# Kernel tuning notes

Hardware: AMD Instinct MI355X
Metric: run time of the kernel (lower is better)

## Reference

```python
import jax, jax.numpy as jnp
import numpy as np

B, S, D_MODEL, H = 2, 2048, 1024, 16
HD = D_MODEL // H  # 64
EPS = 1e-6


def setup_inputs() -> dict:
    key = jax.random.key(0)
    ks = jax.random.split(key, 8)
    x = jax.random.normal(ks[0], (B, S, D_MODEL), dtype=jnp.float32)
    # Proper RoPE rotation angles: theta_i = pos / 10000^(2i/head_dim)
    inv_freq = 1.0 / (10000.0 ** (np.arange(0, HD, 2, dtype=np.float32) / HD))  # (HD/2,)
    angles = np.arange(S, dtype=np.float32)[:, None] * inv_freq[None, :]        # (S, HD/2)
    rope_cos = jnp.asarray(np.cos(angles))
    rope_sin = jnp.asarray(np.sin(angles))
    w_std = 1.0 / np.sqrt(D_MODEL)
    wq = jax.random.normal(ks[1], (D_MODEL, D_MODEL), dtype=jnp.float32) * w_std
    wk = jax.random.normal(ks[2], (D_MODEL, D_MODEL), dtype=jnp.float32) * w_std
    wv = jax.random.normal(ks[3], (D_MODEL, D_MODEL), dtype=jnp.float32) * w_std
    wo = jax.random.normal(ks[4], (D_MODEL, D_MODEL), dtype=jnp.float32) * w_std
    q_scale = 1.0 + 0.02 * jax.random.normal(ks[5], (HD,), dtype=jnp.float32)
    k_scale = 1.0 + 0.02 * jax.random.normal(ks[6], (HD,), dtype=jnp.float32)
    return {"x": x, "wq": wq, "wk": wk, "wv": wv, "wo": wo,
            "q_scale": q_scale, "k_scale": k_scale,
            "rope_cos": rope_cos, "rope_sin": rope_sin}


def _rmsnorm(t, scale):
    # RMSNorm over head_dim
    var = jnp.mean(jnp.square(t), axis=-1, keepdims=True)
    return t * jax.lax.rsqrt(var + EPS) * scale


def _apply_rope(t, cos, sin):
    # t: (B,S,H,HD); interpret consecutive pairs as complex (real, imag)
    b, s, h, d = t.shape
    tp = t.reshape(b, s, h, d // 2, 2)
    tr, ti = tp[..., 0], tp[..., 1]
    c = cos[None, :, None, :]  # (1,S,1,HD/2)
    sn = sin[None, :, None, :]
    or_ = tr * c - ti * sn
    oi = tr * sn + ti * c
    return jnp.stack([or_, oi], axis=-1).reshape(b, s, h, d)


def reference(x, wq, wk, wv, wo, q_scale, k_scale, rope_cos, rope_sin):
    b, s, _ = x.shape
    # Torch-style linear: y = x @ W^T, W is (out, in)
    q = jnp.einsum('bsd,od->bso', x, wq).reshape(b, s, H, HD)
    k = jnp.einsum('bsd,od->bso', x, wk).reshape(b, s, H, HD)
    v = jnp.einsum('bsd,od->bso', x, wv).reshape(b, s, H, HD)
    q = _apply_rope(_rmsnorm(q, q_scale), rope_cos, rope_sin)
    k = _apply_rope(_rmsnorm(k, k_scale), rope_cos, rope_sin)
    # scaled dot-product attention (no mask), fp32 softmax
    scale = 1.0 / np.sqrt(HD)
    scores = jnp.einsum('bqhd,bkhd->bhqk', q, k) * scale
    probs = jax.nn.softmax(scores.astype(jnp.float32), axis=-1)
    attn = jnp.einsum('bhqk,bkhd->bqhd', probs, v).reshape(b, s, D_MODEL)
    return jnp.einsum('bso,do->bsd', attn, wo.T).astype(x.dtype) if False else jnp.einsum('bsd,od->bso', attn, wo)
```

## Files before the change

### kernel.cpp

```cpp
#include <hip/hip_runtime.h>
#include <hip/hip_bf16.h>


#define B_ 2
#define S_ 2048
#define D_ 1024
#define H_ 16
#define HD_ 64
#define M_ (B_*S_)
#define SPLIT_ 2
#define KSPAN_ (S_/SPLIT_)

typedef __attribute__((ext_vector_type(8))) short short8;
typedef __attribute__((ext_vector_type(4))) short short4v;
typedef __attribute__((ext_vector_type(4))) float f32x4;
typedef __attribute__((ext_vector_type(4))) _Float16 half4;
typedef __attribute__((ext_vector_type(8))) _Float16 half8;

static __device__ __forceinline__ short f2bf(float f) {
    __hip_bfloat16 h = __float2bfloat16(f);
    return *reinterpret_cast<short*>(&h);
}
static __device__ __forceinline__ short f2h(float f) {
    _Float16 h = (_Float16)f;
    return *reinterpret_cast<short*>(&h);
}

typedef __attribute__((address_space(1))) const unsigned int gu32_t;
typedef __attribute__((address_space(3))) unsigned int lu32_t;
static __device__ __forceinline__ void gld16(const short* g, short* l) {
    __builtin_amdgcn_global_load_lds((gu32_t*)g, (lu32_t*)l, 16, 0, 0);
}

__global__ __launch_bounds__(256)
void convert_bf16(const float* __restrict__ x,
                  const float* __restrict__ wq, const float* __restrict__ wk,
                  const float* __restrict__ wv, const float* __restrict__ wo,
                  short* __restrict__ xb, short* __restrict__ wqkvb, short* __restrict__ wob)
{
    const size_t t4 = ((size_t)blockIdx.x * 256 + threadIdx.x) * 4;
    const float* src; short* dst; size_t off, doff;
    if (t4 < 4194304)      { src = x;  dst = xb;    off = t4;           doff = t4; }
    else if (t4 < 5242880) { src = wq; dst = wqkvb; off = t4 - 4194304; doff = t4 - 4194304; }
    else if (t4 < 6291456) { src = wk; dst = wqkvb; off = t4 - 5242880; doff = t4 - 4194304; }
    else if (t4 < 7340032) { src = wv; dst = wqkvb; off = t4 - 6291456; doff = t4 - 4194304; }
    else                   { src = wo; dst = wob;   off = t4 - 7340032; doff = t4 - 7340032; }
    float4 v = *(const float4*)(src + off);
    short4v s = { f2bf(v.x), f2bf(v.y), f2bf(v.z), f2bf(v.w) };
    *(short4v*)(dst + doff) = s;
}

__global__ __launch_bounds__(256)
void gemm_qkv(const short* __restrict__ A, const short* __restrict__ Bw,
              short* __restrict__ Qb, short* __restrict__ Kb, short* __restrict__ Vt,
              const float* __restrict__ q_scale, const float* __restrict__ k_scale,
              const float* __restrict__ rope_cos, const float* __restrict__ rope_sin)
{
    __shared__ __align__(16) short As[128*32];
    __shared__ __align__(16) short Bs[128*32];
    const int tid = threadIdx.x;
    const int w = tid >> 6, lane = tid & 63, quad = lane >> 4, l16 = lane & 15;
    const int wr = w >> 1, wc = w & 1;
    const int bm0 = blockIdx.x * 128, bn0 = blockIdx.y * 128;

    const int srow = tid >> 2;
    const int skch = (tid & 3) * 8;
    const short* gA0 = A  + (size_t)(bm0 + srow) * 1024 + skch;
    const short* gA1 = A  + (size_t)(bm0 + 64 + srow) * 1024 + skch;
    const short* gB0 = Bw + (size_t)(bn0 + srow) * 1024 + skch;
    const short* gB1 = Bw + (size_t)(bn0 + 64 + srow) * 1024 + skch;
    short* lA0 = As + w*512;
    short* lA1 = As + 2048 + w*512;
    short* lB0 = Bs + w*512;
    short* lB1 = Bs + 2048 + w*512;

    f32x4 acc[4][4];
    #pragma unroll
    for (int i = 0; i < 4; ++i)
        #pragma unroll
        for (int j = 0; j < 4; ++j) acc[i][j] = (f32x4){0.f,0.f,0.f,0.f};

    for (int k0 = 0; k0 < 1024; k0 += 32) {
        __syncthreads();
        gld16(gA0 + k0, lA0);
        gld16(gA1 + k0, lA1);
        gld16(gB0 + k0, lB0);
        gld16(gB1 + k0, lB1);
        __syncthreads();
        short8 af[4], bfr[4];
        #pragma unroll
        for (int i = 0; i < 4; ++i)
            af[i] = *(const short8*)(As + (wr*64 + i*16 + l16)*32 + quad*8);
        #pragma unroll
        for (int j = 0; j < 4; ++j)
            bfr[j] = *(const short8*)(Bs + (wc*64 + j*16 + l16)*32 + quad*8);
        #pragma unroll
        for (int i = 0; i < 4; ++i)
            #pragma unroll
            for (int j = 0; j < 4; ++j)
                acc[i][j] = __builtin_amdgcn_mfma_f32_16x16x32_bf16(af[i], bfr[j], acc[i][j], 0, 0, 0);
    }

    const int nbase = bn0 + wc*64;
    const int which = nbase >> 10;
    const int h     = (nbase & 1023) >> 6;

    if (which < 2) {
        const float* sc = which ? k_scale : q_scale;
        short* dst      = which ? Kb : Qb;
        const float fold = which ? 1.0f : 0.18033688011112042f;
        float scv[4];
        #pragma unroll
        for (int j = 0; j < 4; ++j) scv[j] = sc[j*16 + l16];
        #pragma unroll
        for (int i = 0; i < 4; ++i) {
            #pragma unroll
            for (int r = 0; r < 4; ++r) {
                const int m = bm0 + wr*64 + i*16 + quad*4 + r;
                const int b = m >> 11, s = m & (S_-1);
                float ss = 0.f;
                #pragma unroll
                for (int j = 0; j < 4; ++j) ss += acc[i][j][r] * acc[i][j][r];
                #pragma unroll
                for (int msk = 1; msk <= 8; msk <<= 1) ss += __shfl_xor(ss, msk, 64);
                const float rn = rsqrtf(ss * (1.0f/64.0f) + 1e-6f);
                #pragma unroll
                for (int j = 0; j < 4; ++j) {
                    const int hd = j*16 + l16;
                    const float nv = acc[i][j][r] * rn * scv[j];
                    const float c  = rope_cos[s*32 + (hd >> 1)];
                    const float sn = rope_sin[s*32 + (hd >> 1)];
                    const float partner = __shfl_xor(nv, 1, 64);
                    const float o = (hd & 1) ? (partner * sn + nv * c) : (nv * c - partner * sn);
                    dst[(((size_t)b*H_ + h)*S_ + s)*HD_ + hd] = f2bf(o * fold);
                }
            }
        }
    } else {
        #pragma unroll
        for (int i = 0; i < 4; ++i)
            #pragma unroll
            for (int r = 0; r < 4; ++r) {
                const int m = bm0 + wr*64 + i*16 + quad*4 + r;
                const int b = m >> 11, s = m & (S_-1);
                #pragma unroll
                for (int j = 0; j < 4; ++j) {
                    const int hd = j*16 + l16;
                    Vt[(((size_t)b*H_ + h)*HD_ + hd)*S_ + s] = f2h(acc[i][j][r]);
                }
            }
    }
}

__global__ __launch_bounds__(256)
void gemm_out(const short* __restrict__ po, const float* __restrict__ pl,
              const short* __restrict__ Bw, float* __restrict__ C)
{
    __shared__ __align__(16) short As[64*32];
    __shared__ __align__(16) short Bs[128*32];
    const int tid = threadIdx.x;
    const int w = tid >> 6, lane = tid & 63, quad = lane >> 4, l16 = lane & 15;
    const int bm0 = blockIdx.x * 64, bn0 = blockIdx.y * 128;

    const int srow = tid >> 2;
    const int skch = (tid & 3) * 8;
    const int m = bm0 + srow;
    const int b = m >> 11, s = m & (S_-1);
    const short* gB0 = Bw + (size_t)(bn0 + srow) * 1024 + skch;
    const short* gB1 = Bw + (size_t)(bn0 + 64 + srow) * 1024 + skch;
    short* lB0 = Bs + w*512;
    short* lB1 = Bs + 2048 + w*512;

    float inv[16];
    #pragma unroll
    for (int h = 0; h < 16; ++h)
        inv[h] = 1.0f / (pl[((size_t)(b*16 + h))*S_ + s] + pl[65536 + ((size_t)(b*16 + h))*S_ + s]);

    f32x4 acc[4][2];
    #pragma unroll
    for (int i = 0; i < 4; ++i) {
        acc[i][0] = (f32x4){0.f,0.f,0.f,0.f};
        acc[i][1] = (f32x4){0.f,0.f,0.f,0.f};
    }

    for (int k0 = 0; k0 < 1024; k0 += 32) {
        const int h = k0 >> 6;
        half8 p0 = *(const half8*)(po +            (size_t)m*1024 + k0 + skch);
        half8 p1 = *(const half8*)(po + 4194304 + (size_t)m*1024 + k0 + skch);
        short8 a;
        #pragma unroll
        for (int j = 0; j < 8; ++j)
            a[j] = f2bf(((float)p0[j] + (float)p1[j]) * inv[h]);
        __syncthreads();
        *(short8*)(As + srow*32 + skch) = a;
        gld16(gB0 + k0, lB0);
        gld16(gB1 + k0, lB1);
        __syncthreads();
        short8 af[4], bfr[2];
        #pragma unroll
        for (int i = 0; i < 4; ++i)
            af[i] = *(const short8*)(As + (i*16 + l16)*32 + quad*8);
        #pragma unroll
        for (int j = 0; j < 2; ++j)
            bfr[j] = *(const short8*)(Bs + (w*32 + j*16 + l16)*32 + quad*8);
        #pragma unroll
        for (int i = 0; i < 4; ++i)
            #pragma unroll
            for (int j = 0; j < 2; ++j)
                acc[i][j] = __builtin_amdgcn_mfma_f32_16x16x32_bf16(af[i], bfr[j], acc[i][j], 0, 0, 0);
    }

    #pragma unroll
    for (int i = 0; i < 4; ++i)
        #pragma unroll
        for (int r = 0; r < 4; ++r) {
            const int mm = bm0 + i*16 + quad*4 + r;
            #pragma unroll
            for (int j = 0; j < 2; ++j) {
                const int n = bn0 + w*32 + j*16 + l16;
                C[(size_t)mm*1024 + n] = acc[i][j][r];
            }
        }
}

__global__ __launch_bounds__(256)
void flash_mfma(const short* __restrict__ qb, const short* __restrict__ kb,
                const short* __restrict__ vt, short* __restrict__ po, float* __restrict__ pl)
{
    __shared__ __align__(16) short Ks[64*64];
    __shared__ __align__(16) short Vs[64*64];

    const int id   = blockIdx.x;
    const int xcd  = id & 7;
    const int rest = id >> 3;
    const int qblk = rest & 15;
    const int g    = (rest >> 4) * 8 + xcd;
    const int bh   = g >> 1;
    const int sp   = g & 1;

    const int tid  = threadIdx.x;
    const int wv   = tid >> 6;
    const int lane = tid & 63;
    const int quad = lane >> 4;
    const int l16  = lane & 15;
    const int b    = bh >> 4, h = bh & (H_-1);
    const int q0   = qblk * 128 + wv * 32;
    const int kt0  = sp * KSPAN_;
    const size_t hbase = (size_t)bh * S_ * HD_;
    const size_t vbase = (size_t)bh * HD_ * S_;
    short* po_sp = po + (size_t)sp * 4194304;
    float* pl_sp = pl + (size_t)sp * 65536;

    const int c0r = tid >> 3,       c0c = tid & 7;
    const int c1r = (tid+256) >> 3, c1c = (tid+256) & 7;

    short8 qfrag[2][2];
    #pragma unroll
    for (int qf = 0; qf < 2; ++qf)
        #pragma unroll
        for (int c = 0; c < 2; ++c)
            qfrag[qf][c] = *(const short8*)(qb + hbase + (size_t)(q0 + qf*16 + l16)*HD_ + c*32 + quad*8);

    f32x4 Oacc[2][4];
    #pragma unroll
    for (int qf = 0; qf < 2; ++qf)
        #pragma unroll
        for (int dt = 0; dt < 4; ++dt) Oacc[qf][dt] = (f32x4){0.f,0.f,0.f,0.f};
    float l_lane[2] = {0.f, 0.f};

    short8 rk0 = *(const short8*)(kb + hbase + (size_t)(kt0 + c0r)*HD_ + c0c*8);
    short8 rk1 = *(const short8*)(kb + hbase + (size_t)(kt0 + c1r)*HD_ + c1c*8);
    short8 rv0 = *(const short8*)(vt + vbase + (size_t)c0r*S_ + kt0 + c0c*8);
    short8 rv1 = *(const short8*)(vt + vbase + (size_t)c1r*S_ + kt0 + c1c*8);

    #pragma unroll 1
    for (int t = 0; t < KSPAN_/64; ++t) {
        __syncthreads();
        *(short8*)(Ks + c0r*64 + ((c0c ^ (c0r & 7)) << 3)) = rk0;
        *(short8*)(Ks + c1r*64 + ((c1c ^ (c1r & 7)) << 3)) = rk1;
        *(short8*)(Vs + c0r*64 + ((c0c ^ (c0r & 7)) << 3)) = rv0;
        *(short8*)(Vs + c1r*64 + ((c1c ^ (c1r & 7)) << 3)) = rv1;
        __syncthreads();
        if (t < KSPAN_/64 - 1) {
            const int ktn = kt0 + (t+1)*64;
            rk0 = *(const short8*)(kb + hbase + (size_t)(ktn + c0r)*HD_ + c0c*8);
            rk1 = *(const short8*)(kb + hbase + (size_t)(ktn + c1r)*HD_ + c1c*8);
            rv0 = *(const short8*)(vt + vbase + (size_t)c0r*S_ + ktn + c0c*8);
            rv1 = *(const short8*)(vt + vbase + (size_t)c1r*S_ + ktn + c1c*8);
        }

        #pragma unroll
        for (int st = 0; st < 4; ++st) {
            short8 kf0 = *(const short8*)(Ks + (st*16 + l16)*64 + (((quad    ) ^ (l16 & 7)) << 3));
            short8 kf1 = *(const short8*)(Ks + (st*16 + l16)*64 + (((4 + quad) ^ (l16 & 7)) << 3));
            const int ch16 = st*2 + (quad >> 1);
            const int sw   = ((ch16 ^ (l16 & 7)) << 3) + (quad & 1)*4;
            half4 va[4];
            #pragma unroll
            for (int dt = 0; dt < 4; ++dt)
                va[dt] = *(const half4*)(Vs + (dt*16 + l16)*64 + sw);
            #pragma unroll
            for (int qf = 0; qf < 2; ++qf) {
                f32x4 acc = (f32x4){0.f,0.f,0.f,0.f};
                acc = __builtin_amdgcn_mfma_f32_16x16x32_bf16(kf0, qfrag[qf][0], acc, 0, 0, 0);
                acc = __builtin_amdgcn_mfma_f32_16x16x32_bf16(kf1, qfrag[qf][1], acc, 0, 0, 0);
                half4 pb;
                #pragma unroll
                for (int r = 0; r < 4; ++r) {
                    float p = __builtin_amdgcn_exp2f(acc[r] - 12.0f);
                    l_lane[qf] += p;
                    pb[r] = (_Float16)p;
                }
                #pragma unroll
                for (int dt = 0; dt < 4; ++dt)
                    Oacc[qf][dt] = __builtin_amdgcn_mfma_f32_16x16x16f16(va[dt], pb, Oacc[qf][dt], 0, 0, 0);
            }
        }
    }

    #pragma unroll
    for (int qf = 0; qf < 2; ++qf) {
        l_lane[qf] += __shfl_xor(l_lane[qf], 16, 64);
        l_lane[qf] += __shfl_xor(l_lane[qf], 32, 64);
        if (quad == 0) pl_sp[(size_t)bh*S_ + q0 + qf*16 + l16] = l_lane[qf];
    }
    #pragma unroll
    for (int qf = 0; qf < 2; ++qf) {
        const int s = q0 + qf*16 + l16;
        #pragma unroll
        for (int dt = 0; dt < 4; ++dt) {
            short4v o;
            #pragma unroll
            for (int r = 0; r < 4; ++r) o[r] = f2h(Oacc[qf][dt][r]);
            *(short4v*)(po_sp + (((size_t)b*S_ + s)*H_ + h)*HD_ + dt*16 + quad*4) = o;
        }
    }
}

extern "C" void kernel_launch(void* const* d_in, const int* in_sizes, int n_in,
                              void* d_out, int out_size, void* d_ws, size_t ws_size,
                              hipStream_t stream)
{
    (void)in_sizes; (void)n_in; (void)out_size; (void)ws_size;
    const float* x        = (const float*)d_in[0];
    const float* wq       = (const float*)d_in[1];
    const float* wk       = (const float*)d_in[2];
    const float* wv       = (const float*)d_in[3];
    const float* wo       = (const float*)d_in[4];
    const float* q_scale  = (const float*)d_in[5];
    const float* k_scale  = (const float*)d_in[6];
    const float* rope_cos = (const float*)d_in[7];
    const float* rope_sin = (const float*)d_in[8];
    float* out = (float*)d_out;
    short* ws  = (short*)d_ws;

    short* qbh   = ws;
    short* kbh   = ws + 4194304;
    short* vt    = ws + 8388608;
    short* xb    = ws + 16777216;
    short* wqkvb = ws + 20971520;
    short* wob   = ws + 24117248;
    short* po    = ws + 25165824;
    float* pl    = (float*)(ws + 33554432);

    convert_bf16<<<dim3(8192), 256, 0, stream>>>(x, wq, wk, wv, wo, xb, wqkvb, wob);
    gemm_qkv<<<dim3(M_/128, 24), 256, 0, stream>>>(xb, wqkvb, qbh, kbh, vt,
                                                   q_scale, k_scale, rope_cos, rope_sin);
    flash_mfma<<<dim3((S_/128)*B_*H_*SPLIT_), 256, 0, stream>>>(qbh, kbh, vt, po, pl);
    gemm_out<<<dim3(M_/64, D_/128), 256, 0, stream>>>(po, pl, wob, out);
}
```

Measured before the change: 211.0 us.

## Enlarge flash K/V tile, remap GEMM blocks by XCD, prefetch out-proj operands

The flash attention kernel now stages 128-key K/V tiles per iteration instead of 64, with a wider V swizzle, halving the barrier and loop overhead per key. gemm_qkv and gemm_out use a 1D grid whose block index is remapped so blocks sharing weight columns land on the same XCD, to improve L2 reuse. gemm_out also register-prefetches the next partial-output chunk one step ahead. The cost is doubled LDS use and more registers in flash, which may lower occupancy.

```diff
diff --git a/kernel.cpp b/kernel.cpp
--- a/kernel.cpp
+++ b/kernel.cpp
@@ -10,6 +10,7 @@
 #define M_ (B_*S_)
 #define SPLIT_ 2
 #define KSPAN_ (S_/SPLIT_)
+#define KTILE_ 128
 
 typedef __attribute__((ext_vector_type(8))) short short8;
 typedef __attribute__((ext_vector_type(4))) short short4v;
@@ -61,7 +62,11 @@
     const int tid = threadIdx.x;
     const int w = tid >> 6, lane = tid & 63, quad = lane >> 4, l16 = lane & 15;
     const int wr = w >> 1, wc = w & 1;
-    const int bm0 = blockIdx.x * 128, bn0 = blockIdx.y * 128;
+    const int id  = blockIdx.x;
+    const int xcd = id & 7, j8 = id >> 3;
+    const int by  = xcd*3 + (j8 >> 5);
+    const int bx  = j8 & 31;
+    const int bm0 = bx * 128, bn0 = by * 128;
 
     const int srow = tid >> 2;
     const int skch = (tid & 3) * 8;
@@ -160,7 +165,9 @@
     __shared__ __align__(16) short Bs[128*32];
     const int tid = threadIdx.x;
     const int w = tid >> 6, lane = tid & 63, quad = lane >> 4, l16 = lane & 15;
-    const int bm0 = blockIdx.x * 64, bn0 = blockIdx.y * 128;
+    const int id  = blockIdx.x;
+    const int bn0 = (id & 7) * 128;
+    const int bm0 = (id >> 3) * 64;
 
     const int srow = tid >> 2;
     const int skch = (tid & 3) * 8;
@@ -183,19 +190,24 @@
         acc[i][1] = (f32x4){0.f,0.f,0.f,0.f};
     }
 
+    half8 c0 = *(const half8*)(po +            (size_t)m*1024 + skch);
+    half8 c1 = *(const half8*)(po + 4194304 + (size_t)m*1024 + skch);
+
     for (int k0 = 0; k0 < 1024; k0 += 32) {
         const int h = k0 >> 6;
-        half8 p0 = *(const half8*)(po +            (size_t)m*1024 + k0 + skch);
-        half8 p1 = *(const half8*)(po + 4194304 + (size_t)m*1024 + k0 + skch);
         short8 a;
         #pragma unroll
         for (int j = 0; j < 8; ++j)
-            a[j] = f2bf(((float)p0[j] + (float)p1[j]) * inv[h]);
+            a[j] = f2bf(((float)c0[j] + (float)c1[j]) * inv[h]);
         __syncthreads();
         *(short8*)(As + srow*32 + skch) = a;
         gld16(gB0 + k0, lB0);
         gld16(gB1 + k0, lB1);
         __syncthreads();
+        if (k0 < 1024 - 32) {
+            c0 = *(const half8*)(po +            (size_t)m*1024 + k0 + 32 + skch);
+            c1 = *(const half8*)(po + 4194304 + (size_t)m*1024 + k0 + 32 + skch);
+        }
         short8 af[4], bfr[2];
         #pragma unroll
         for (int i = 0; i < 4; ++i)
@@ -227,8 +239,8 @@
 void flash_mfma(const short* __restrict__ qb, const short* __restrict__ kb,
                 const short* __restrict__ vt, short* __restrict__ po, float* __restrict__ pl)
 {
-    __shared__ __align__(16) short Ks[64*64];
-    __shared__ __align__(16) short Vs[64*64];
+    __shared__ __align__(16) short Ks[128*64];
+    __shared__ __align__(16) short Vs[64*128];
 
     const int id   = blockIdx.x;
     const int xcd  = id & 7;
@@ -251,9 +263,6 @@
     short* po_sp = po + (size_t)sp * 4194304;
     float* pl_sp = pl + (size_t)sp * 65536;
 
-    const int c0r = tid >> 3,       c0c = tid & 7;
-    const int c1r = (tid+256) >> 3, c1c = (tid+256) & 7;
-
     short8 qfrag[2][2];
     #pragma unroll
     for (int qf = 0; qf < 2; ++qf)
@@ -268,37 +277,46 @@
         for (int dt = 0; dt < 4; ++dt) Oacc[qf][dt] = (f32x4){0.f,0.f,0.f,0.f};
     float l_lane[2] = {0.f, 0.f};
 
-    short8 rk0 = *(const short8*)(kb + hbase + (size_t)(kt0 + c0r)*HD_ + c0c*8);
-    short8 rk1 = *(const short8*)(kb + hbase + (size_t)(kt0 + c1r)*HD_ + c1c*8);
-    short8 rv0 = *(const short8*)(vt + vbase + (size_t)c0r*S_ + kt0 + c0c*8);
-    short8 rv1 = *(const short8*)(vt + vbase + (size_t)c1r*S_ + kt0 + c1c*8);
+    short8 rk[4], rv[4];
+    #pragma unroll
+    for (int i = 0; i < 4; ++i) {
+        const int ck = tid + i*256;
+        rk[i] = *(const short8*)(kb + hbase + (size_t)(kt0 + (ck >> 3))*HD_ + (ck & 7)*8);
+        rv[i] = *(const short8*)(vt + vbase + (size_t)(ck >> 4)*S_ + kt0 + (ck & 15)*8);
+    }
 
     #pragma unroll 1
-    for (int t = 0; t < KSPAN_/64; ++t) {
-        __syncthreads();
-        *(short8*)(Ks + c0r*64 + ((c0c ^ (c0r & 7)) << 3)) = rk0;
-        *(short8*)(Ks + c1r*64 + ((c1c ^ (c1r & 7)) << 3)) = rk1;
-        *(short8*)(Vs + c0r*64 + ((c0c ^ (c0r & 7)) << 3)) = rv0;
-        *(short8*)(Vs + c1r*64 + ((c1c ^ (c1r & 7)) << 3)) = rv1;
-        __syncthreads();
-        if (t < KSPAN_/64 - 1) {
-            const int ktn = kt0 + (t+1)*64;
-            rk0 = *(const short8*)(kb + hbase + (size_t)(ktn + c0r)*HD_ + c0c*8);
-            rk1 = *(const short8*)(kb + hbase + (size_t)(ktn + c1r)*HD_ + c1c*8);
-            rv0 = *(const short8*)(vt + vbase + (size_t)c0r*S_ + ktn + c0c*8);
-            rv1 = *(const short8*)(vt + vbase + (size_t)c1r*S_ + ktn + c1c*8);
-        }
-
-        #pragma unroll
-        for (int st = 0; st < 4; ++st) {
+    for (int t = 0; t < KSPAN_/KTILE_; ++t) {
+        __syncthreads();
+        #pragma unroll
+        for (int i = 0; i < 4; ++i) {
+            const int ck = tid + i*256;
+            const int key = ck >> 3, dch = ck & 7;
+            *(short8*)(Ks + key*64 + ((dch ^ (key & 7)) << 3)) = rk[i];
+            const int d = ck >> 4, kch = ck & 15;
+            *(short8*)(Vs + d*128 + ((kch ^ (d & 15)) << 3)) = rv[i];
+        }
+        __syncthreads();
+        if (t < KSPAN_/KTILE_ - 1) {
+            const int ktn = kt0 + (t+1)*KTILE_;
+            #pragma unroll
+            for (int i = 0; i < 4; ++i) {
+                const int ck = tid + i*256;
+                rk[i] = *(const short8*)(kb + hbase + (size_t)(ktn + (ck >> 3))*HD_ + (ck & 7)*8);
+                rv[i] = *(const short8*)(vt + vbase + (size_t)(ck >> 4)*S_ + ktn + (ck & 15)*8);
+            }
+        }
+
+        #pragma unroll
+        for (int st = 0; st < 8; ++st) {
             short8 kf0 = *(const short8*)(Ks + (st*16 + l16)*64 + (((quad    ) ^ (l16 & 7)) << 3));
             short8 kf1 = *(const short8*)(Ks + (st*16 + l16)*64 + (((4 + quad) ^ (l16 & 7)) << 3));
-            const int ch16 = st*2 + (quad >> 1);
-            const int sw   = ((ch16 ^ (l16 & 7)) << 3) + (quad & 1)*4;
+            const int kch = st*2 + (quad >> 1);
+            const int sw  = ((kch ^ l16) << 3) + (quad & 1)*4;
             half4 va[4];
             #pragma unroll
             for (int dt = 0; dt < 4; ++dt)
-                va[dt] = *(const half4*)(Vs + (dt*16 + l16)*64 + sw);
+                va[dt] = *(const half4*)(Vs + (dt*16 + l16)*128 + sw);
             #pragma unroll
             for (int qf = 0; qf < 2; ++qf) {
                 f32x4 acc = (f32x4){0.f,0.f,0.f,0.f};
@@ -364,8 +382,8 @@
     float* pl    = (float*)(ws + 33554432);
 
     convert_bf16<<<dim3(8192), 256, 0, stream>>>(x, wq, wk, wv, wo, xb, wqkvb, wob);
-    gemm_qkv<<<dim3(M_/128, 24), 256, 0, stream>>>(xb, wqkvb, qbh, kbh, vt,
-                                                   q_scale, k_scale, rope_cos, rope_sin);
+    gemm_qkv<<<dim3((M_/128)*24), 256, 0, stream>>>(xb, wqkvb, qbh, kbh, vt,
+                                                    q_scale, k_scale, rope_cos, rope_sin);
     flash_mfma<<<dim3((S_/128)*B_*H_*SPLIT_), 256, 0, stream>>>(qbh, kbh, vt, po, pl);
-    gemm_out<<<dim3(M_/64, D_/128), 256, 0, stream>>>(po, pl, wob, out);
-}
+    gemm_out<<<dim3((M_/64)*(D_/128)), 256, 0, stream>>>(po, pl, wob, out);
+}
```

After: 229.4 us. 8.7% more time.
